# Kernel tuning notes

Measured on AMD Instinct MI355X. Metric: run time of the kernel, lower is better.

## Reference

```python
import jax, jax.numpy as jnp
import numpy as np

EPS = 1e-5
CROSS = 12  # cross_size


def bn(x, g, b):
    # inference BatchNorm2d with running_mean=0, running_var=1
    s = g / jnp.sqrt(1.0 + EPS)
    return x * s[None, :, None, None] + b[None, :, None, None]


def conv1x1(x, w, b=None):
    # w: [out_c, in_c]
    y = jnp.einsum('bchw,oc->bohw', x, w)
    if b is not None:
        y = y + b[None, :, None, None]
    return y


def mlp(x, w1, b1, w2, b2):
    # Mlp with channels_first=True: 1x1 conv -> GELU -> 1x1 conv (drop=0)
    return conv1x1(jax.nn.gelu(conv1x1(x, w1, b1), approximate=False), w2, b2)


def setup_inputs() -> dict:
    key = jax.random.key(0)
    ks = jax.random.split(key, 24)
    B, Cl, Ch = 8, 128, 64
    Hl = Wl = 96
    Hh = Wh = 192

    def w(k, o, i):
        return jax.random.normal(k, (o, i), jnp.float32) / np.float32(np.sqrt(i))

    return {
        'x_l': jax.random.normal(ks[0], (B, Cl, Hl, Wl), jnp.float32),
        'x_h': jax.random.normal(ks[1], (B, Ch, Hh, Wh), jnp.float32),
        # mlp_l (hidden = in = Cl)
        'mlp_l_w1': w(ks[2], Cl, Cl), 'mlp_l_b1': jnp.zeros((Cl,), jnp.float32),
        'mlp_l_w2': w(ks[3], Cl, Cl), 'mlp_l_b2': jnp.zeros((Cl,), jnp.float32),
        # conv_1x1(Cl->Ch) + BN + ReLU
        'conv_w': w(ks[4], Ch, Cl),
        'conv_bn_g': jnp.ones((Ch,), jnp.float32), 'conv_bn_b': jnp.zeros((Ch,), jnp.float32),
        # cross_kv: BN(Cl) -> AdaptiveMaxPool(12,12) -> Conv1x1(Cl -> 2*Ch)
        'kv_bn_g': jnp.ones((Cl,), jnp.float32), 'kv_bn_b': jnp.zeros((Cl,), jnp.float32),
        'kv_w': w(ks[5], 2 * Ch, Cl), 'kv_b': jnp.zeros((2 * Ch,), jnp.float32),
        # self.norm: BN(Ch)
        'norm_g': jnp.ones((Ch,), jnp.float32), 'norm_b': jnp.zeros((Ch,), jnp.float32),
        # mlp_h
        'mlp_h_w1': w(ks[6], Ch, Ch), 'mlp_h_b1': jnp.zeros((Ch,), jnp.float32),
        'mlp_h_w2': w(ks[7], Ch, Ch), 'mlp_h_b2': jnp.zeros((Ch,), jnp.float32),
    }


def reference(x_l, x_h,
              mlp_l_w1, mlp_l_b1, mlp_l_w2, mlp_l_b2,
              conv_w, conv_bn_g, conv_bn_b,
              kv_bn_g, kv_bn_b, kv_w, kv_b,
              norm_g, norm_b,
              mlp_h_w1, mlp_h_b1, mlp_h_w2, mlp_h_b2):
    B, Cl, Hl, Wl = x_l.shape
    _, Ch, Hh, Wh = x_h.shape
    S = CROSS * CROSS  # 144

    # x_l = x_l + mlp_l(x_l)
    x_l = x_l + mlp(x_l, mlp_l_w1, mlp_l_b1, mlp_l_w2, mlp_l_b2)

    # x_h = x_h + interpolate(conv(x_l))
    x_l_conv = jax.nn.relu(bn(conv1x1(x_l, conv_w), conv_bn_g, conv_bn_b))
    up = jax.image.resize(x_l_conv, (B, Ch, Hh, Wh), method='linear')
    x_h = x_h + up

    # cross_kv(x_l): BN -> adaptive max pool to 12x12 -> 1x1 conv to 2*Ch
    xn_l = bn(x_l, kv_bn_g, kv_bn_b)
    pooled = xn_l.reshape(B, Cl, CROSS, Hl // CROSS, CROSS, Wl // CROSS).max(axis=(3, 5))
    kv = conv1x1(pooled, kv_w, kv_b)              # [B, 2*Ch, 12, 12]
    k, v = kv[:, :Ch], kv[:, Ch:]                 # each [B, Ch, 12, 12]
    k_mat = k.transpose(0, 2, 3, 1).reshape(B, S, Ch)  # grouped-conv kernel [B,S,Ch]
    v_mat = v.reshape(B, Ch, S)                        # grouped-conv kernel [B,Ch,S]

    # attn_h
    xn_h = bn(x_h, norm_g, norm_b)                # [B,Ch,Hh,Wh]
    attn = jnp.einsum('bchw,bsc->bshw', xn_h, k_mat)  # [B,S,Hh,Wh]
    attn = jax.nn.softmax(attn * (S ** -0.5), axis=1)
    out = jnp.einsum('bshw,bcs->bchw', attn, v_mat)   # [B,Ch,Hh,Wh]
    x_h = x_h + out

    # x_h = x_h + mlp_h(x_h)
    x_h = x_h + mlp(x_h, mlp_h_w1, mlp_h_b1, mlp_h_w2, mlp_h_b2)
    return x_h
```

## Files before the change

### kernel.cpp

```cpp
#include <hip/hip_runtime.h>
#include <math.h>

#define NB 8
#define CL 128
#define CH 64
#define HL 96
#define WL 96
#define PL (HL*WL)
#define HH 192
#define WH 192
#define PH (HH*WH)
#define NS 144
#define BN_S 0.9999950000374997f
#define INV12 (1.0f/12.0f)

typedef __attribute__((ext_vector_type(8))) short bf16x8;
typedef __attribute__((ext_vector_type(4))) float f32x4;
typedef __attribute__((ext_vector_type(2))) unsigned int uu2;
#define MFMA16(a,b,c) __builtin_amdgcn_mfma_f32_16x16x32_bf16(a,b,c,0,0,0)

__device__ __forceinline__ float gelu_exact(float x){
    return 0.5f*x*(1.0f + erff(x*0.7071067811865475f));
}
__device__ __forceinline__ short f2bf(float f){
    union { float f; unsigned u; } v; v.f = f;
    unsigned r = v.u + 0x7FFFu + ((v.u >> 16) & 1u);
    return (short)(r >> 16);
}
__device__ __forceinline__ void st4(short* p, float a, float b, float c, float d){
    uu2 r;
    asm("v_cvt_pk_bf16_f32 %0, %1, %2" : "=v"(r.x) : "v"(a), "v"(b));
    asm("v_cvt_pk_bf16_f32 %0, %1, %2" : "=v"(r.y) : "v"(c), "v"(d));
    *(uu2*)p = r;
}
__device__ __forceinline__ void st4v(short* p, float4 v){ st4(p, v.x, v.y, v.z, v.w); }

__global__ __launch_bounds__(256) void k_mlp_l(
    const float* __restrict__ xl, const float* __restrict__ w1, const float* __restrict__ b1,
    const float* __restrict__ w2, const float* __restrict__ b2,
    const float* __restrict__ cw, const float* __restrict__ bng, const float* __restrict__ bnb,
    float* __restrict__ xl2, float* __restrict__ xc)
{
    __shared__ short Wb[128*136];
    __shared__ short Xb[64*136];
    __shared__ float bS[256];
    __shared__ float bC[128];
    const int tid = threadIdx.x;
    const int b   = blockIdx.x / (PL/64);
    const int hw0 = (blockIdx.x % (PL/64)) * 64;
    const float* xb = xl + (size_t)b*CL*PL + hw0;
    #pragma unroll
    for (int i=0;i<16;i++){
        int idx4 = i*256+tid;
        int row = idx4>>5, c4 = (idx4&31)<<2;
        st4v(&Wb[row*136 + c4], *(const float4*)&w1[(row<<7) + c4]);
    }
    {
        const int p = tid&63, wv = tid>>6;
        #pragma unroll
        for (int i=0;i<8;i++){
            int c0 = wv*4 + i*16;
            float a0 = xb[(size_t)(c0+0)*PL + p];
            float a1 = xb[(size_t)(c0+1)*PL + p];
            float a2 = xb[(size_t)(c0+2)*PL + p];
            float a3 = xb[(size_t)(c0+3)*PL + p];
            st4(&Xb[p*136 + c0], a0,a1,a2,a3);
        }
    }
    if (tid < 128) bS[tid] = b1[tid]; else bS[tid] = b2[tid-128];
    __syncthreads();
    const int w = tid>>6, lane = tid&63, l16 = lane&15, q = lane>>4;
    const int pw = w*16, px = pw + l16;
    float hv[8][4];
    #pragma unroll
    for (int mt=0; mt<8; mt++){
        f32x4 acc = {0.f,0.f,0.f,0.f};
        #pragma unroll
        for (int k=0;k<4;k++){
            bf16x8 af = *(const bf16x8*)&Wb[(mt*16+l16)*136 + k*32 + q*8];
            bf16x8 bf = *(const bf16x8*)&Xb[(pw+l16)*136 + k*32 + q*8];
            acc = MFMA16(af, bf, acc);
        }
        #pragma unroll
        for (int r=0;r<4;r++) hv[mt][r] = gelu_exact(acc[r] + bS[mt*16+q*4+r]);
    }
    #pragma unroll
    for (int mt=0;mt<8;mt++)
        st4(&Xb[px*136 + mt*16 + q*4], hv[mt][0],hv[mt][1],hv[mt][2],hv[mt][3]);
    __syncthreads();
    #pragma unroll
    for (int i=0;i<16;i++){
        int idx4 = i*256+tid;
        int row = idx4>>5, c4 = (idx4&31)<<2;
        st4v(&Wb[row*136 + c4], *(const float4*)&w2[(row<<7) + c4]);
    }
    __syncthreads();
    float* yb = xl2 + (size_t)b*CL*PL + hw0;
    #pragma unroll
    for (int mt=0; mt<8; mt++){
        f32x4 acc = {0.f,0.f,0.f,0.f};
        #pragma unroll
        for (int k=0;k<4;k++){
            bf16x8 af = *(const bf16x8*)&Wb[(mt*16+l16)*136 + k*32 + q*8];
            bf16x8 bf = *(const bf16x8*)&Xb[(pw+l16)*136 + k*32 + q*8];
            acc = MFMA16(af, bf, acc);
        }
        #pragma unroll
        for (int r=0;r<4;r++){
            int o = mt*16 + q*4 + r;
            size_t off = (size_t)o*PL + px;
            float yy = acc[r] + bS[128+o] + xb[off];
            yb[off] = yy;
            hv[mt][r] = yy;
        }
    }
    #pragma unroll
    for (int mt=0;mt<8;mt++)
        st4(&Xb[px*136 + mt*16 + q*4], hv[mt][0],hv[mt][1],hv[mt][2],hv[mt][3]);
    __syncthreads();
    #pragma unroll
    for (int i=0;i<8;i++){
        int idx4 = i*256+tid;
        int row = idx4>>5, c4 = (idx4&31)<<2;
        st4v(&Wb[row*136 + c4], *(const float4*)&cw[(row<<7) + c4]);
    }
    if (tid < 64) bC[tid] = bng[tid]*BN_S; else if (tid < 128) bC[tid] = bnb[tid-64];
    __syncthreads();
    float* cb = xc + (size_t)b*CH*PL + hw0;
    #pragma unroll
    for (int mt=0; mt<4; mt++){
        f32x4 acc = {0.f,0.f,0.f,0.f};
        #pragma unroll
        for (int k=0;k<4;k++){
            bf16x8 af = *(const bf16x8*)&Wb[(mt*16+l16)*136 + k*32 + q*8];
            bf16x8 bf = *(const bf16x8*)&Xb[(pw+l16)*136 + k*32 + q*8];
            acc = MFMA16(af, bf, acc);
        }
        #pragma unroll
        for (int r=0;r<4;r++){
            int o = mt*16 + q*4 + r;
            cb[(size_t)o*PL + px] = fmaxf(bC[o]*acc[r] + bC[64+o], 0.f);
        }
    }
}

__global__ __launch_bounds__(192) void k_pool(
    const float* __restrict__ xl2, const float* __restrict__ g, const float* __restrict__ bta,
    float* __restrict__ pooled)
{
    const int plane = blockIdx.x;
    const int tid = threadIdx.x;
    if (tid >= NS) return;
    const int c = plane & (CL-1);
    const float sc = g[c]*BN_S;
    const float tc = bta[c];
    const int i = tid/12, j = tid%12;
    const float* base = xl2 + (size_t)plane*PL + (size_t)i*8*WL + j*8;
    float m = -3.4e38f;
    #pragma unroll
    for (int dy=0;dy<8;dy++){
        const float* rr = base + dy*WL;
        #pragma unroll
        for (int dx=0;dx<8;dx++) m = fmaxf(m, sc*rr[dx]+tc);
    }
    pooled[(size_t)plane*NS + tid] = m;
}

__global__ __launch_bounds__(256) void k_kv(
    const float* __restrict__ pooled, const float* __restrict__ kvw, const float* __restrict__ kvb,
    const float* __restrict__ ng, const float* __restrict__ nb,
    float* __restrict__ keg, float* __restrict__ vg, float* __restrict__ biasg)
{
    const int t = blockIdx.x*256 + threadIdx.x;
    const int s = t % NS;
    const int r = t / NS;
    const int o = r & 127;
    const int b = r >> 7;
    const float* P = pooled + (size_t)b*CL*NS + s;
    const float* W = kvw + (size_t)o*CL;
    float acc = kvb[o];
    #pragma unroll 4
    for (int c=0;c<CL;c++) acc = fmaf(W[c], P[(size_t)c*NS], acc);
    if (o < CH){
        keg[((size_t)b*NS+s)*CH + o] = acc * (ng[o]*(BN_S*INV12));
        atomicAdd(&biasg[b*NS+s], acc * (nb[o]*INV12));
    } else {
        vg[((size_t)b*CH + (o-CH))*NS + s] = acc;
    }
}

__global__ __launch_bounds__(256) void k_attn(
    const float* __restrict__ xh, const float* __restrict__ xc,
    const float* __restrict__ keg, const float* __restrict__ vg,
    const float* __restrict__ biasg,
    const float* __restrict__ w1h, const float* __restrict__ b1h,
    const float* __restrict__ w2h, const float* __restrict__ b2h,
    float* __restrict__ out)
{
    __shared__ short KP[144*72];
    __shared__ short VW[64*160];
    __shared__ short Xb[64*72];
    __shared__ float bS[NS];
    __shared__ float bH[128];
    const int tid = threadIdx.x;
    const int b   = blockIdx.x / (PH/64);
    const int hw0 = (blockIdx.x % (PH/64)) * 64;
    const int y   = hw0 / WH;
    const int xst = hw0 % WH;
    const int   lyr = (y>>1) - ((y&1)^1);
    const float fy  = (y&1) ? 0.25f : 0.75f;
    const int   y0i = lyr<0?0:lyr;
    const int   y1i = (lyr+1>HL-1)?(HL-1):(lyr+1);

    const float* xb  = xh + (size_t)b*CH*PH + hw0;
    const float* xcb = xc + (size_t)b*CH*PL;
    const float* keb = keg + (size_t)b*NS*CH;
    const float* vb  = vg + (size_t)b*CH*NS;

    const int w = tid>>6, lane = tid&63, l16 = lane&15, q = lane>>4;
    const int pw = w*16, px = pw + l16;

    #pragma unroll
    for (int i=0;i<9;i++){
        int idx4 = i*256+tid;
        int s = idx4>>4, c4 = (idx4&15)<<2;
        st4v(&KP[s*72 + c4], *(const float4*)&keb[(s<<6) + c4]);
    }
    #pragma unroll
    for (int i=0;i<9;i++){
        int idx4 = i*256+tid;
        int c = idx4/36, s4 = (idx4 - c*36)<<2;
        st4v(&VW[c*160 + s4], *(const float4*)&vb[c*NS + s4]);
    }
    { int row = tid>>2, o4 = (tid&3)<<2;
      *(uu2*)&VW[row*160 + 144 + o4] = (uu2){0u,0u}; }
    if (tid < NS) bS[tid] = biasg[b*NS+tid];
    if (tid < 64) bH[tid] = b1h[tid]; else if (tid < 128) bH[tid] = b2h[tid-64];

    const int xo  = xst + px;
    const int lx  = (xo>>1) - ((xo&1)^1);
    const float fx = (xo&1) ? 0.25f : 0.75f;
    const int x0i = lx<0?0:lx;
    const int x1i = (lx+1>WL-1)?(WL-1):(lx+1);
    float resid[16];
    #pragma unroll
    for (int mt=0; mt<4; mt++){
        #pragma unroll
        for (int r=0; r<4; r++){
            int ch = mt*16 + q*4 + r;
            const float* s = xcb + (size_t)ch*PL;
            float v00 = s[y0i*WL+x0i], v01 = s[y0i*WL+x1i];
            float v10 = s[y1i*WL+x0i], v11 = s[y1i*WL+x1i];
            float top = v00 + fx*(v01-v00);
            float bot = v10 + fx*(v11-v10);
            float up  = top + fy*(bot-top);
            resid[mt*4+r] = xb[(size_t)ch*PH + px] + up;
        }
        st4(&Xb[px*72 + mt*16 + q*4],
            resid[mt*4+0], resid[mt*4+1], resid[mt*4+2], resid[mt*4+3]);
    }
    __syncthreads();

    float ev[9][4];
    float mloc = -3.4e38f;
    #pragma unroll
    for (int st=0; st<9; st++){
        f32x4 acc = {0.f,0.f,0.f,0.f};
        #pragma unroll
        for (int k=0;k<2;k++){
            bf16x8 af = *(const bf16x8*)&KP[(st*16+l16)*72 + k*32 + q*8];
            bf16x8 bf = *(const bf16x8*)&Xb[(pw+l16)*72 + k*32 + q*8];
            acc = MFMA16(af, bf, acc);
        }
        #pragma unroll
        for (int r=0;r<4;r++){
            float v = acc[r] + bS[st*16+q*4+r];
            ev[st][r] = v; mloc = fmaxf(mloc, v);
        }
    }
    mloc = fmaxf(mloc, __shfl_xor(mloc,16));
    mloc = fmaxf(mloc, __shfl_xor(mloc,32));
    float sloc = 0.f;
    #pragma unroll
    for (int st=0;st<9;st++)
        #pragma unroll
        for (int r=0;r<4;r++){ float e = __expf(ev[st][r]-mloc); ev[st][r]=e; sloc+=e; }
    sloc += __shfl_xor(sloc,16);
    sloc += __shfl_xor(sloc,32);
    const float rs = 1.f/sloc;
    __syncthreads();

    #pragma unroll
    for (int st=0;st<9;st++)
        st4(&KP[px*160 + st*16 + q*4], ev[st][0], ev[st][1], ev[st][2], ev[st][3]);
    *(uu2*)&KP[px*160 + 144 + q*4] = (uu2){0u,0u};

    #pragma unroll
    for (int mt=0; mt<4; mt++){
        f32x4 acc = {0.f,0.f,0.f,0.f};
        #pragma unroll
        for (int k=0;k<5;k++){
            bf16x8 af = *(const bf16x8*)&VW[(mt*16+l16)*160 + k*32 + q*8];
            bf16x8 bf = *(const bf16x8*)&KP[(pw+l16)*160 + k*32 + q*8];
            acc = MFMA16(af, bf, acc);
        }
        #pragma unroll
        for (int r=0;r<4;r++)
            resid[mt*4+r] = resid[mt*4+r] + acc[r]*rs;
        st4(&Xb[px*72 + mt*16 + q*4],
            resid[mt*4+0], resid[mt*4+1], resid[mt*4+2], resid[mt*4+3]);
    }
    __syncthreads();

    #pragma unroll
    for (int i=0;i<4;i++){
        int idx4 = i*256+tid;
        int o = idx4>>4, c4 = (idx4&15)<<2;
        st4v(&VW[o*72 + c4], *(const float4*)&w1h[(o<<6) + c4]);
    }
    #pragma unroll
    for (int i=0;i<4;i++){
        int idx4 = i*256+tid;
        int o = idx4>>4, c4 = (idx4&15)<<2;
        st4v(&VW[4608 + o*72 + c4], *(const float4*)&w2h[(o<<6) + c4]);
    }
    __syncthreads();

    float hv[4][4];
    #pragma unroll
    for (int mt=0; mt<4; mt++){
        f32x4 acc = {0.f,0.f,0.f,0.f};
        #pragma unroll
        for (int k=0;k<2;k++){
            bf16x8 af = *(const bf16x8*)&VW[(mt*16+l16)*72 + k*32 + q*8];
            bf16x8 bf = *(const bf16x8*)&Xb[(pw+l16)*72 + k*32 + q*8];
            acc = MFMA16(af, bf, acc);
        }
        #pragma unroll
        for (int r=0;r<4;r++) hv[mt][r] = gelu_exact(acc[r] + bH[mt*16+q*4+r]);
    }
    #pragma unroll
    for (int mt=0;mt<4;mt++)
        st4(&Xb[px*72 + mt*16 + q*4], hv[mt][0], hv[mt][1], hv[mt][2], hv[mt][3]);

    float* ob = out + (size_t)b*CH*PH + hw0;
    #pragma unroll
    for (int mt=0; mt<4; mt++){
        f32x4 acc = {0.f,0.f,0.f,0.f};
        #pragma unroll
        for (int k=0;k<2;k++){
            bf16x8 af = *(const bf16x8*)&VW[4608 + (mt*16+l16)*72 + k*32 + q*8];
            bf16x8 bf = *(const bf16x8*)&Xb[(pw+l16)*72 + k*32 + q*8];
            acc = MFMA16(af, bf, acc);
        }
        #pragma unroll
        for (int r=0;r<4;r++){
            int ch = mt*16 + q*4 + r;
            ob[(size_t)ch*PH + px] = acc[r] + bH[64+ch] + resid[mt*4+r];
        }
    }
}

extern "C" void kernel_launch(void* const* d_in, const int* in_sizes, int n_in,
                              void* d_out, int out_size, void* d_ws, size_t ws_size,
                              hipStream_t stream)
{
    const float* xl    = (const float*)d_in[0];
    const float* xh    = (const float*)d_in[1];
    const float* ml_w1 = (const float*)d_in[2];
    const float* ml_b1 = (const float*)d_in[3];
    const float* ml_w2 = (const float*)d_in[4];
    const float* ml_b2 = (const float*)d_in[5];
    const float* cw    = (const float*)d_in[6];
    const float* cbg   = (const float*)d_in[7];
    const float* cbb   = (const float*)d_in[8];
    const float* kbg   = (const float*)d_in[9];
    const float* kbb   = (const float*)d_in[10];
    const float* kvw   = (const float*)d_in[11];
    const float* kvb   = (const float*)d_in[12];
    const float* ng    = (const float*)d_in[13];
    const float* nb    = (const float*)d_in[14];
    const float* mh_w1 = (const float*)d_in[15];
    const float* mh_b1 = (const float*)d_in[16];
    const float* mh_w2 = (const float*)d_in[17];
    const float* mh_b2 = (const float*)d_in[18];
    float* out = (float*)d_out;

    float* ws     = (float*)d_ws;
    float* xl2    = ws;
    float* xc     = xl2    + (size_t)NB*CL*PL;
    float* pooled = xc     + (size_t)NB*CH*PL;
    float* keg    = pooled + (size_t)NB*CL*NS;
    float* vg     = keg    + (size_t)NB*NS*CH;
    float* biasg  = vg     + (size_t)NB*NS*CH;

    k_mlp_l<<<dim3(NB*PL/64), dim3(256), 0, stream>>>(xl, ml_w1, ml_b1, ml_w2, ml_b2,
                                                      cw, cbg, cbb, xl2, xc);
    k_pool<<<dim3(NB*CL), dim3(192), 0, stream>>>(xl2, kbg, kbb, pooled);
    hipMemsetAsync(biasg, 0, (size_t)NB*NS*sizeof(float), stream);
    k_kv<<<dim3((NB*128*NS)/256), dim3(256), 0, stream>>>(pooled, kvw, kvb, ng, nb, keg, vg, biasg);
    k_attn<<<dim3(NB*PH/64), dim3(256), 0, stream>>>(xh, xc, keg, vg, biasg,
                                                     mh_w1, mh_b1, mh_w2, mh_b2, out);
}
```

Baseline: 310.7 us.

## Load small MLP and conv weights straight into registers, dropping LDS staging barriers

The conv_1x1 weights in k_mlp_l and the mlp_h weights in k_attn are now read from global memory straight into MFMA A-fragment registers, converted to bf16 on the fly. This removes the LDS staging passes for those weights and two __syncthreads pairs. It also vectorises the max-pool loads with float4 and changes the KP/VW LDS row pitch to 168 to reduce bank conflicts. In exchange the kernels hold more VGPRs, which may lower occupancy, and each wave reads the weights from global/L2 on its own.

```diff
diff --git a/kernel.cpp b/kernel.cpp
--- a/kernel.cpp
+++ b/kernel.cpp
@@ -22,11 +22,6 @@
 __device__ __forceinline__ float gelu_exact(float x){
     return 0.5f*x*(1.0f + erff(x*0.7071067811865475f));
 }
-__device__ __forceinline__ short f2bf(float f){
-    union { float f; unsigned u; } v; v.f = f;
-    unsigned r = v.u + 0x7FFFu + ((v.u >> 16) & 1u);
-    return (short)(r >> 16);
-}
 __device__ __forceinline__ void st4(short* p, float a, float b, float c, float d){
     uu2 r;
     asm("v_cvt_pk_bf16_f32 %0, %1, %2" : "=v"(r.x) : "v"(a), "v"(b));
@@ -34,6 +29,16 @@
     *(uu2*)p = r;
 }
 __device__ __forceinline__ void st4v(short* p, float4 v){ st4(p, v.x, v.y, v.z, v.w); }
+__device__ __forceinline__ bf16x8 ld8bf(const float* p){
+    float4 a = *(const float4*)p;
+    float4 b = *(const float4*)(p+4);
+    union { unsigned u[4]; bf16x8 v; } r;
+    asm("v_cvt_pk_bf16_f32 %0, %1, %2" : "=v"(r.u[0]) : "v"(a.x), "v"(a.y));
+    asm("v_cvt_pk_bf16_f32 %0, %1, %2" : "=v"(r.u[1]) : "v"(a.z), "v"(a.w));
+    asm("v_cvt_pk_bf16_f32 %0, %1, %2" : "=v"(r.u[2]) : "v"(b.x), "v"(b.y));
+    asm("v_cvt_pk_bf16_f32 %0, %1, %2" : "=v"(r.u[3]) : "v"(b.z), "v"(b.w));
+    return r.v;
+}
 
 __global__ __launch_bounds__(256) void k_mlp_l(
     const float* __restrict__ xl, const float* __restrict__ w1, const float* __restrict__ b1,
@@ -49,6 +54,8 @@
     const int b   = blockIdx.x / (PL/64);
     const int hw0 = (blockIdx.x % (PL/64)) * 64;
     const float* xb = xl + (size_t)b*CL*PL + hw0;
+    const int w = tid>>6, lane = tid&63, l16 = lane&15, q = lane>>4;
+    const int pw = w*16, px = pw + l16;
     #pragma unroll
     for (int i=0;i<16;i++){
         int idx4 = i*256+tid;
@@ -68,9 +75,8 @@
         }
     }
     if (tid < 128) bS[tid] = b1[tid]; else bS[tid] = b2[tid-128];
+    if (tid < 64) bC[tid] = bng[tid]*BN_S; else if (tid < 128) bC[tid] = bnb[tid-64];
     __syncthreads();
-    const int w = tid>>6, lane = tid&63, l16 = lane&15, q = lane>>4;
-    const int pw = w*16, px = pw + l16;
     float hv[8][4];
     #pragma unroll
     for (int mt=0; mt<8; mt++){
@@ -95,6 +101,12 @@
         st4v(&Wb[row*136 + c4], *(const float4*)&w2[(row<<7) + c4]);
     }
     __syncthreads();
+    bf16x8 cwf[4][4];
+    #pragma unroll
+    for (int mt=0; mt<4; mt++)
+        #pragma unroll
+        for (int k=0;k<4;k++)
+            cwf[mt][k] = ld8bf(cw + (size_t)(mt*16+l16)*128 + k*32 + q*8);
     float* yb = xl2 + (size_t)b*CL*PL + hw0;
     #pragma unroll
     for (int mt=0; mt<8; mt++){
@@ -117,24 +129,14 @@
     #pragma unroll
     for (int mt=0;mt<8;mt++)
         st4(&Xb[px*136 + mt*16 + q*4], hv[mt][0],hv[mt][1],hv[mt][2],hv[mt][3]);
-    __syncthreads();
-    #pragma unroll
-    for (int i=0;i<8;i++){
-        int idx4 = i*256+tid;
-        int row = idx4>>5, c4 = (idx4&31)<<2;
-        st4v(&Wb[row*136 + c4], *(const float4*)&cw[(row<<7) + c4]);
-    }
-    if (tid < 64) bC[tid] = bng[tid]*BN_S; else if (tid < 128) bC[tid] = bnb[tid-64];
-    __syncthreads();
     float* cb = xc + (size_t)b*CH*PL + hw0;
     #pragma unroll
     for (int mt=0; mt<4; mt++){
         f32x4 acc = {0.f,0.f,0.f,0.f};
         #pragma unroll
         for (int k=0;k<4;k++){
-            bf16x8 af = *(const bf16x8*)&Wb[(mt*16+l16)*136 + k*32 + q*8];
             bf16x8 bf = *(const bf16x8*)&Xb[(pw+l16)*136 + k*32 + q*8];
-            acc = MFMA16(af, bf, acc);
+            acc = MFMA16(cwf[mt][k], bf, acc);
         }
         #pragma unroll
         for (int r=0;r<4;r++){
@@ -159,9 +161,11 @@
     float m = -3.4e38f;
     #pragma unroll
     for (int dy=0;dy<8;dy++){
-        const float* rr = base + dy*WL;
-        #pragma unroll
-        for (int dx=0;dx<8;dx++) m = fmaxf(m, sc*rr[dx]+tc);
+        float4 a = *(const float4*)(base + dy*WL);
+        float4 bb = *(const float4*)(base + dy*WL + 4);
+        float m0 = fmaxf(fmaxf(sc*a.x+tc, sc*a.y+tc), fmaxf(sc*a.z+tc, sc*a.w+tc));
+        float m1 = fmaxf(fmaxf(sc*bb.x+tc, sc*bb.y+tc), fmaxf(sc*bb.z+tc, sc*bb.w+tc));
+        m = fmaxf(m, fmaxf(m0, m1));
     }
     pooled[(size_t)plane*NS + tid] = m;
 }
@@ -197,8 +201,8 @@
     const float* __restrict__ w2h, const float* __restrict__ b2h,
     float* __restrict__ out)
 {
-    __shared__ short KP[144*72];
-    __shared__ short VW[64*160];
+    __shared__ short KP[64*168];
+    __shared__ short VW[64*168];
     __shared__ short Xb[64*72];
     __shared__ float bS[NS];
     __shared__ float bH[128];
@@ -230,12 +234,18 @@
     for (int i=0;i<9;i++){
         int idx4 = i*256+tid;
         int c = idx4/36, s4 = (idx4 - c*36)<<2;
-        st4v(&VW[c*160 + s4], *(const float4*)&vb[c*NS + s4]);
+        st4v(&VW[c*168 + s4], *(const float4*)&vb[c*NS + s4]);
     }
     { int row = tid>>2, o4 = (tid&3)<<2;
-      *(uu2*)&VW[row*160 + 144 + o4] = (uu2){0u,0u}; }
+      *(uu2*)&VW[row*168 + 144 + o4] = (uu2){0u,0u}; }
     if (tid < NS) bS[tid] = biasg[b*NS+tid];
     if (tid < 64) bH[tid] = b1h[tid]; else if (tid < 128) bH[tid] = b2h[tid-64];
+    bf16x8 w1f[4][2];
+    #pragma unroll
+    for (int mt=0; mt<4; mt++)
+        #pragma unroll
+        for (int k=0;k<2;k++)
+            w1f[mt][k] = ld8bf(w1h + (size_t)(mt*16+l16)*64 + k*32 + q*8);
 
     const int xo  = xst + px;
     const int lx  = (xo>>1) - ((xo&1)^1);
@@ -290,18 +300,25 @@
     const float rs = 1.f/sloc;
     __syncthreads();
 
+    bf16x8 w2f[4][2];
+    #pragma unroll
+    for (int mt=0; mt<4; mt++)
+        #pragma unroll
+        for (int k=0;k<2;k++)
+            w2f[mt][k] = ld8bf(w2h + (size_t)(mt*16+l16)*64 + k*32 + q*8);
+
     #pragma unroll
     for (int st=0;st<9;st++)
-        st4(&KP[px*160 + st*16 + q*4], ev[st][0], ev[st][1], ev[st][2], ev[st][3]);
-    *(uu2*)&KP[px*160 + 144 + q*4] = (uu2){0u,0u};
+        st4(&KP[px*168 + st*16 + q*4], ev[st][0], ev[st][1], ev[st][2], ev[st][3]);
+    *(uu2*)&KP[px*168 + 144 + q*4] = (uu2){0u,0u};
 
     #pragma unroll
     for (int mt=0; mt<4; mt++){
         f32x4 acc = {0.f,0.f,0.f,0.f};
         #pragma unroll
         for (int k=0;k<5;k++){
-            bf16x8 af = *(const bf16x8*)&VW[(mt*16+l16)*160 + k*32 + q*8];
-            bf16x8 bf = *(const bf16x8*)&KP[(pw+l16)*160 + k*32 + q*8];
+            bf16x8 af = *(const bf16x8*)&VW[(mt*16+l16)*168 + k*32 + q*8];
+            bf16x8 bf = *(const bf16x8*)&KP[(pw+l16)*168 + k*32 + q*8];
             acc = MFMA16(af, bf, acc);
         }
         #pragma unroll
@@ -310,21 +327,6 @@
         st4(&Xb[px*72 + mt*16 + q*4],
             resid[mt*4+0], resid[mt*4+1], resid[mt*4+2], resid[mt*4+3]);
     }
-    __syncthreads();
-
-    #pragma unroll
-    for (int i=0;i<4;i++){
-        int idx4 = i*256+tid;
-        int o = idx4>>4, c4 = (idx4&15)<<2;
-        st4v(&VW[o*72 + c4], *(const float4*)&w1h[(o<<6) + c4]);
-    }
-    #pragma unroll
-    for (int i=0;i<4;i++){
-        int idx4 = i*256+tid;
-        int o = idx4>>4, c4 = (idx4&15)<<2;
-        st4v(&VW[4608 + o*72 + c4], *(const float4*)&w2h[(o<<6) + c4]);
-    }
-    __syncthreads();
 
     float hv[4][4];
     #pragma unroll
@@ -332,9 +334,8 @@
         f32x4 acc = {0.f,0.f,0.f,0.f};
         #pragma unroll
         for (int k=0;k<2;k++){
-            bf16x8 af = *(const bf16x8*)&VW[(mt*16+l16)*72 + k*32 + q*8];
             bf16x8 bf = *(const bf16x8*)&Xb[(pw+l16)*72 + k*32 + q*8];
-            acc = MFMA16(af, bf, acc);
+            acc = MFMA16(w1f[mt][k], bf, acc);
         }
         #pragma unroll
         for (int r=0;r<4;r++) hv[mt][r] = gelu_exact(acc[r] + bH[mt*16+q*4+r]);
@@ -349,9 +350,8 @@
         f32x4 acc = {0.f,0.f,0.f,0.f};
         #pragma unroll
         for (int k=0;k<2;k++){
-            bf16x8 af = *(const bf16x8*)&VW[4608 + (mt*16+l16)*72 + k*32 + q*8];
             bf16x8 bf = *(const bf16x8*)&Xb[(pw+l16)*72 + k*32 + q*8];
-            acc = MFMA16(af, bf, acc);
+            acc = MFMA16(w2f[mt][k], bf, acc);
         }
         #pragma unroll
         for (int r=0;r<4;r++){
```

Result: slower. 433.3 us (+39.5%).
